# Kernel optimization log

Hardware: AMD Instinct MI355X
Metric: run time of the kernel (lower is better)

The kernel has to match this reference:

```python
import jax, jax.numpy as jnp
import numpy as np

NP_, NL_ = 2048, 128          # protein / ligand node counts
D_IN, D_OUT, NUM_HEAD = 128, 128, 1
NEG_SLOPE, EPS = 0.2, 1e-10


def setup_inputs() -> dict:
    key = jax.random.key(0)
    k1, k2, k3, k4 = jax.random.split(key, 4)
    node_feat_protein = jax.random.normal(k1, (NP_, D_IN), jnp.float32)
    node_feat_ligand = jax.random.normal(k2, (NL_, D_IN), jnp.float32)
    W = jax.random.normal(k3, (D_IN, D_OUT), jnp.float32) / np.sqrt(D_IN)
    b = jnp.zeros((D_OUT,), jnp.float32)
    query = jax.random.normal(k4, (NUM_HEAD, 2 * D_OUT // NUM_HEAD), jnp.float32) * 0.1
    # full bipartite cross-graph edges, both directions (as in get_graph_intra)
    ip = jnp.repeat(jnp.arange(NP_, dtype=jnp.int32), NL_)          # [Np*Nl]
    il = jnp.tile(jnp.arange(NL_, dtype=jnp.int32) + NP_, NP_)      # [Np*Nl]
    node_in = jnp.concatenate([ip, il])
    node_out = jnp.concatenate([il, ip])
    edge_list = jnp.stack([node_in, node_out], axis=1)              # [2*Np*Nl, 2]
    return {"node_feat_protein": node_feat_protein,
            "node_feat_ligand": node_feat_ligand,
            "edge_list": edge_list,
            "W": W, "b": b, "query": query}


def _gat_forward(node_feat, edge_list, W, b, query):
    N = node_feat.shape[0]
    H = query.shape[0]
    # add self-loops (torchdrug GraphAttentionConv.message)
    self_idx = jnp.arange(N, dtype=edge_list.dtype)
    node_in = jnp.concatenate([edge_list[:, 0], self_idx])
    node_out = jnp.concatenate([edge_list[:, 1], self_idx])
    E = node_in.shape[0]

    hidden = node_feat @ W + b                                  # [N, D_OUT]
    h_in = hidden[node_in]                                      # [E, D_OUT]
    h_out = hidden[node_out]                                    # [E, D_OUT]
    # key = [h_in ; h_out] split into heads
    key_eh = jnp.concatenate([h_in, h_out], axis=-1).reshape(E, H, -1)
    logits = jnp.einsum("hd,ehd->eh", query, key_eh)            # [E, H]
    logits = jax.nn.leaky_relu(logits, NEG_SLOPE)
    # segment softmax over destination nodes (every node has a self-loop)
    seg_max = jax.ops.segment_max(logits, node_out, num_segments=N)
    att = jnp.exp(logits - seg_max[node_out])                   # edge_weight == 1
    seg_sum = jax.ops.segment_sum(att, node_out, num_segments=N)
    att = att / (seg_sum[node_out] + EPS)                       # [E, H]

    value = h_in.reshape(E, H, -1)                              # [E, H, D/H]
    message = (att[..., None] * value).reshape(E, -1)           # [E, D_OUT]
    update = jax.ops.segment_sum(message, node_out, num_segments=N)
    return jax.nn.relu(update)                                  # default activation


def reference(node_feat_protein, node_feat_ligand, edge_list, W, b, query):
    node_feat = jnp.concatenate([node_feat_protein, node_feat_ligand])
    out = _gat_forward(node_feat, edge_list, W, b, query)
    n_p = node_feat_protein.shape[0]
    return out[:n_p], out[n_p:]
```

## Files before the change

kernel.cpp:

```cpp
#include <hip/hip_runtime.h>
#include <math.h>


#define NP 2048
#define NL 128
#define NN 2176

static __device__ float g_hidden[NN * 128];
static __device__ float g_ain[NN];
static __device__ float g_aout[NN];
static __device__ float g_part[16 * 128 * 128];
static __device__ float g_einvL[NL];

__device__ __forceinline__ float lrelu(float x) { return x > 0.f ? x : 0.2f * x; }

__global__ void k1_hidden(const float* xp, const float* xl, const float* W,
                          const float* b, const float* q)
{
    __shared__ float Xs[16][128];
    const int tid = threadIdx.x;
    const int cg = tid & 31;
    const int rs = tid >> 5;
    const int base = blockIdx.x * 16;

    for (int t = tid; t < 512; t += 256) {
        int flat = t * 4, row = flat >> 7, col = flat & 127;
        int n = base + row;
        const float* src = (n < NP) ? (xp + n * 128) : (xl + (n - NP) * 128);
        *(float4*)&Xs[row][col] = *(const float4*)(src + col);
    }
    __syncthreads();

    const int r0 = rs * 2, r1 = r0 + 1;
    float4 bv = *(const float4*)(b + cg * 4);
    float4 a0 = bv, a1 = bv;
    #pragma unroll 8
    for (int k = 0; k < 128; ++k) {
        float4 w4 = *(const float4*)(W + k * 128 + cg * 4);
        float x0 = Xs[r0][k], x1 = Xs[r1][k];
        a0.x = fmaf(x0, w4.x, a0.x); a0.y = fmaf(x0, w4.y, a0.y);
        a0.z = fmaf(x0, w4.z, a0.z); a0.w = fmaf(x0, w4.w, a0.w);
        a1.x = fmaf(x1, w4.x, a1.x); a1.y = fmaf(x1, w4.y, a1.y);
        a1.z = fmaf(x1, w4.z, a1.z); a1.w = fmaf(x1, w4.w, a1.w);
    }
    *(float4*)(g_hidden + (base + r0) * 128 + cg * 4) = a0;
    *(float4*)(g_hidden + (base + r1) * 128 + cg * 4) = a1;

    float4 q1v = *(const float4*)(q + cg * 4);
    float4 q2v = *(const float4*)(q + 128 + cg * 4);
    float p10 = q1v.x*a0.x + q1v.y*a0.y + q1v.z*a0.z + q1v.w*a0.w;
    float p20 = q2v.x*a0.x + q2v.y*a0.y + q2v.z*a0.z + q2v.w*a0.w;
    float p11 = q1v.x*a1.x + q1v.y*a1.y + q1v.z*a1.z + q1v.w*a1.w;
    float p21 = q2v.x*a1.x + q2v.y*a1.y + q2v.z*a1.z + q2v.w*a1.w;
    #pragma unroll
    for (int off = 16; off; off >>= 1) {
        p10 += __shfl_xor(p10, off); p20 += __shfl_xor(p20, off);
        p11 += __shfl_xor(p11, off); p21 += __shfl_xor(p21, off);
    }
    if (cg == 0) {
        g_ain[base + r0] = p10; g_aout[base + r0] = p20;
        g_ain[base + r1] = p11; g_aout[base + r1] = p21;
    }
}

__global__ void k2_attn(float* out)
{
    __shared__ float Hl[128 * 64];
    __shared__ __align__(16) float wsl[4][128];
    __shared__ float As[NP];
    __shared__ __align__(16) float ws2[16 * 128];
    __shared__ float sm[16], sinv[16];

    const int tid = threadIdx.x;
    const int bid = blockIdx.x;

    if (bid < 256) {
        const int colbase = (bid & 1) * 64;
        const int pbase = (bid >> 1) * 16;
        for (int t = tid; t < 2048; t += 256) {
            int flat = t * 4, l = flat >> 6, c = flat & 63;
            *(float4*)&Hl[flat] = *(const float4*)(g_hidden + (NP + l) * 128 + colbase + c);
        }
        __syncthreads();

        const int slot = tid >> 6, lane = tid & 63;
        const float ai0 = g_ain[NP + lane];
        const float ai1 = g_ain[NP + 64 + lane];
        for (int pp = 0; pp < 4; ++pp) {
            const int p = pbase + slot * 4 + pp;
            const float ao = g_aout[p];
            const float sl = lrelu(g_ain[p] + ao);
            float lg0 = lrelu(ai0 + ao), lg1 = lrelu(ai1 + ao);
            float m = fmaxf(lg0, lg1);
            #pragma unroll
            for (int off = 32; off; off >>= 1) m = fmaxf(m, __shfl_xor(m, off));
            m = fmaxf(m, sl);
            float e0 = expf(lg0 - m), e1 = expf(lg1 - m);
            float s = e0 + e1;
            #pragma unroll
            for (int off = 32; off; off >>= 1) s += __shfl_xor(s, off);
            float es = expf(sl - m);
            float inv = 1.f / (s + es + 1e-10f);
            wsl[slot][lane] = e0 * inv;
            wsl[slot][lane + 64] = e1 * inv;

            float acc = es * inv * g_hidden[p * 128 + colbase + lane];
            #pragma unroll
            for (int l = 0; l < 128; l += 4) {
                float4 w4 = *(float4*)&wsl[slot][l];
                acc = fmaf(w4.x, Hl[l * 64 + lane], acc);
                acc = fmaf(w4.y, Hl[(l + 1) * 64 + lane], acc);
                acc = fmaf(w4.z, Hl[(l + 2) * 64 + lane], acc);
                acc = fmaf(w4.w, Hl[(l + 3) * 64 + lane], acc);
            }
            out[p * 128 + colbase + lane] = acc > 0.f ? acc : 0.f;
        }
    } else {
        const int lb = bid - 256;
        const int pchunk = lb >> 3, lgroup = lb & 7;
        const int p0 = pchunk * 128, lbase = lgroup * 16;

        for (int t = tid; t < 512; t += 256)
            *(float4*)&As[t * 4] = *(const float4*)(g_ain + t * 4);
        __syncthreads();

        const int li = tid >> 4, tt = tid & 15;
        const int l = lbase + li;
        const float ao = g_aout[NP + l];
        float mx = -1e30f;
        for (int p = tt; p < NP; p += 16)
            mx = fmaxf(mx, lrelu(As[p] + ao));
        #pragma unroll
        for (int off = 8; off; off >>= 1) mx = fmaxf(mx, __shfl_xor(mx, off));
        const float sl = lrelu(g_ain[NP + l] + ao);
        const float m = fmaxf(mx, sl);
        float s = 0.f;
        for (int p = tt; p < NP; p += 16)
            s += expf(lrelu(As[p] + ao) - m);
        #pragma unroll
        for (int off = 8; off; off >>= 1) s += __shfl_xor(s, off);
        const float es = expf(sl - m);
        const float inv = 1.f / (s + es + 1e-10f);
        if (tt == 0) {
            sm[li] = m; sinv[li] = inv;
            if (pchunk == 0) g_einvL[l] = es * inv;
        }
        __syncthreads();

        for (int t = tid; t < 2048; t += 256) {
            int li2 = t >> 7, pi = t & 127;
            float ao2 = g_aout[NP + lbase + li2];
            ws2[t] = expf(lrelu(As[p0 + pi] + ao2) - sm[li2]) * sinv[li2];
        }
        __syncthreads();

        const int cc = tid & 127, lh = tid >> 7;
        float acc[8];
        #pragma unroll
        for (int u = 0; u < 8; ++u) acc[u] = 0.f;
        for (int pi = 0; pi < 128; pi += 4) {
            float h0 = g_hidden[(p0 + pi) * 128 + cc];
            float h1 = g_hidden[(p0 + pi + 1) * 128 + cc];
            float h2 = g_hidden[(p0 + pi + 2) * 128 + cc];
            float h3 = g_hidden[(p0 + pi + 3) * 128 + cc];
            #pragma unroll
            for (int u = 0; u < 8; ++u) {
                float4 w4 = *(float4*)&ws2[(lh * 8 + u) * 128 + pi];
                acc[u] = fmaf(w4.w, h3, fmaf(w4.z, h2,
                         fmaf(w4.y, h1, fmaf(w4.x, h0, acc[u]))));
            }
        }
        #pragma unroll
        for (int u = 0; u < 8; ++u)
            g_part[(pchunk * 128 + lbase + lh * 8 + u) * 128 + cc] = acc[u];
    }
}

__global__ void k3_finish(float* out)
{
    const int idx = blockIdx.x * 256 + threadIdx.x;
    const int l = idx >> 7, c = idx & 127;
    float s = g_einvL[l] * g_hidden[(NP + l) * 128 + c];
    #pragma unroll
    for (int k = 0; k < 16; ++k)
        s += g_part[(k * 128 + l) * 128 + c];
    out[(NP + l) * 128 + c] = s > 0.f ? s : 0.f;
}

extern "C" void kernel_launch(void* const* d_in, const int* in_sizes, int n_in,
                              void* d_out, int out_size, void* d_ws, size_t ws_size,
                              hipStream_t stream) {
    const float* xp = (const float*)d_in[0];
    const float* xl = (const float*)d_in[1];
    const float* W  = (const float*)d_in[3];
    const float* b  = (const float*)d_in[4];
    const float* q  = (const float*)d_in[5];
    float* out = (float*)d_out;

    k1_hidden<<<136, 256, 0, stream>>>(xp, xl, W, b, q);
    k2_attn<<<384, 256, 0, stream>>>(out);
    k3_finish<<<64, 256, 0, stream>>>(out);
}
```

Before: 104.8 us.

## Fuse final ligand reduction into attention kernel via last-block atomic counter

Drops the separate k3_finish launch. Each ligand-group block in k2 now increments a per-group atomic counter, and the last of the 16 blocks sums the partials and writes the ligand output. k1 is also reshaped to one row per thread-row across 272 blocks, doubling parallelism on the 256-CU GPU. The aim is to save a kernel launch and its dependency gap, at the cost of threadfences, atomics and a serialized tail reduction in the last block.

```diff
diff --git a/kernel.cpp b/kernel.cpp
--- a/kernel.cpp
+++ b/kernel.cpp
@@ -9,67 +9,62 @@
 static __device__ float g_hidden[NN * 128];
 static __device__ float g_ain[NN];
 static __device__ float g_aout[NN];
-static __device__ float g_part[16 * 128 * 128];
+static __device__ float g_part[16 * NL * 128];
 static __device__ float g_einvL[NL];
+static __device__ unsigned g_cnt[8];
 
 __device__ __forceinline__ float lrelu(float x) { return x > 0.f ? x : 0.2f * x; }
 
-__global__ void k1_hidden(const float* xp, const float* xl, const float* W,
-                          const float* b, const float* q)
+__global__ __launch_bounds__(256) void k1_hidden(
+    const float* xp, const float* xl, const float* W,
+    const float* b, const float* q)
 {
-    __shared__ float Xs[16][128];
+    __shared__ float Xs[8][128];
     const int tid = threadIdx.x;
+    const int bid = blockIdx.x;
+    if (bid == 0 && tid < 8) g_cnt[tid] = 0;
+
     const int cg = tid & 31;
     const int rs = tid >> 5;
-    const int base = blockIdx.x * 16;
-
-    for (int t = tid; t < 512; t += 256) {
-        int flat = t * 4, row = flat >> 7, col = flat & 127;
+    const int base = bid * 8;
+    {
+        int flat = tid * 4, row = flat >> 7, col = flat & 127;
         int n = base + row;
-        const float* src = (n < NP) ? (xp + n * 128) : (xl + (n - NP) * 128);
+        const float* src = (n < NP) ? xp + n * 128 : xl + (n - NP) * 128;
         *(float4*)&Xs[row][col] = *(const float4*)(src + col);
     }
     __syncthreads();
 
-    const int r0 = rs * 2, r1 = r0 + 1;
-    float4 bv = *(const float4*)(b + cg * 4);
-    float4 a0 = bv, a1 = bv;
+    float4 a = *(const float4*)(b + cg * 4);
     #pragma unroll 8
     for (int k = 0; k < 128; ++k) {
         float4 w4 = *(const float4*)(W + k * 128 + cg * 4);
-        float x0 = Xs[r0][k], x1 = Xs[r1][k];
-        a0.x = fmaf(x0, w4.x, a0.x); a0.y = fmaf(x0, w4.y, a0.y);
-        a0.z = fmaf(x0, w4.z, a0.z); a0.w = fmaf(x0, w4.w, a0.w);
-        a1.x = fmaf(x1, w4.x, a1.x); a1.y = fmaf(x1, w4.y, a1.y);
-        a1.z = fmaf(x1, w4.z, a1.z); a1.w = fmaf(x1, w4.w, a1.w);
-    }
-    *(float4*)(g_hidden + (base + r0) * 128 + cg * 4) = a0;
-    *(float4*)(g_hidden + (base + r1) * 128 + cg * 4) = a1;
+        float x = Xs[rs][k];
+        a.x = fmaf(x, w4.x, a.x); a.y = fmaf(x, w4.y, a.y);
+        a.z = fmaf(x, w4.z, a.z); a.w = fmaf(x, w4.w, a.w);
+    }
+    *(float4*)(g_hidden + (base + rs) * 128 + cg * 4) = a;
 
     float4 q1v = *(const float4*)(q + cg * 4);
     float4 q2v = *(const float4*)(q + 128 + cg * 4);
-    float p10 = q1v.x*a0.x + q1v.y*a0.y + q1v.z*a0.z + q1v.w*a0.w;
-    float p20 = q2v.x*a0.x + q2v.y*a0.y + q2v.z*a0.z + q2v.w*a0.w;
-    float p11 = q1v.x*a1.x + q1v.y*a1.y + q1v.z*a1.z + q1v.w*a1.w;
-    float p21 = q2v.x*a1.x + q2v.y*a1.y + q2v.z*a1.z + q2v.w*a1.w;
+    float p1 = q1v.x*a.x + q1v.y*a.y + q1v.z*a.z + q1v.w*a.w;
+    float p2 = q2v.x*a.x + q2v.y*a.y + q2v.z*a.z + q2v.w*a.w;
     #pragma unroll
     for (int off = 16; off; off >>= 1) {
-        p10 += __shfl_xor(p10, off); p20 += __shfl_xor(p20, off);
-        p11 += __shfl_xor(p11, off); p21 += __shfl_xor(p21, off);
-    }
-    if (cg == 0) {
-        g_ain[base + r0] = p10; g_aout[base + r0] = p20;
-        g_ain[base + r1] = p11; g_aout[base + r1] = p21;
-    }
+        p1 += __shfl_xor(p1, off);
+        p2 += __shfl_xor(p2, off);
+    }
+    if (cg == 0) { g_ain[base + rs] = p1; g_aout[base + rs] = p2; }
 }
 
-__global__ void k2_attn(float* out)
+__global__ __launch_bounds__(256) void k2_attn(float* out)
 {
     __shared__ float Hl[128 * 64];
     __shared__ __align__(16) float wsl[4][128];
     __shared__ float As[NP];
     __shared__ __align__(16) float ws2[16 * 128];
     __shared__ float sm[16], sinv[16];
+    __shared__ int s_last;
 
     const int tid = threadIdx.x;
     const int bid = blockIdx.x;
@@ -173,18 +168,25 @@
         #pragma unroll
         for (int u = 0; u < 8; ++u)
             g_part[(pchunk * 128 + lbase + lh * 8 + u) * 128 + cc] = acc[u];
-    }
-}
-
-__global__ void k3_finish(float* out)
-{
-    const int idx = blockIdx.x * 256 + threadIdx.x;
-    const int l = idx >> 7, c = idx & 127;
-    float s = g_einvL[l] * g_hidden[(NP + l) * 128 + c];
-    #pragma unroll
-    for (int k = 0; k < 16; ++k)
-        s += g_part[(k * 128 + l) * 128 + c];
-    out[(NP + l) * 128 + c] = s > 0.f ? s : 0.f;
+
+        __syncthreads();
+        __threadfence();
+        if (tid == 0)
+            s_last = (atomicAdd(&g_cnt[lgroup], 1u) == 15u) ? 1 : 0;
+        __syncthreads();
+        if (s_last) {
+            __threadfence();
+            for (int t = tid; t < 2048; t += 256) {
+                int li2 = t >> 7, c = t & 127;
+                int l2 = lbase + li2;
+                float sum = g_einvL[l2] * g_hidden[(NP + l2) * 128 + c];
+                #pragma unroll
+                for (int k = 0; k < 16; ++k)
+                    sum += g_part[(k * 128 + l2) * 128 + c];
+                out[(NP + l2) * 128 + c] = sum > 0.f ? sum : 0.f;
+            }
+        }
+    }
 }
 
 extern "C" void kernel_launch(void* const* d_in, const int* in_sizes, int n_in,
@@ -197,7 +199,6 @@
     const float* q  = (const float*)d_in[5];
     float* out = (float*)d_out;
 
-    k1_hidden<<<136, 256, 0, stream>>>(xp, xl, W, b, q);
+    k1_hidden<<<272, 256, 0, stream>>>(xp, xl, W, b, q);
     k2_attn<<<384, 256, 0, stream>>>(out);
-    k3_finish<<<64, 256, 0, stream>>>(out);
 }
```

Result: slower. 117.8 us (+12.4%).
